# Kernel tuning notes

Hardware: AMD Instinct MI355X
Metric: run time of the kernel (lower is better)

## Reference

```python
import jax, jax.numpy as jnp
import numpy as np

V = 100000   # vocab (emb_size == stoich_size so all 8 branches index safely)
D = 256      # emb_dimension
S = 128      # stoich_dimension
H = 512      # hidden_size
B = 8192     # batch of skip-gram pairs
K = 32       # negative samples per pair
NUM_REGULAR = 60000  # num_regular_words


def _mlp(x, w1, b1, w2, b2):
    # Sequential(Linear(S,H), ReLU, Linear(H,D))
    return jax.nn.relu(x @ w1 + b1) @ w2 + b2


def setup_inputs() -> dict:
    key = jax.random.key(0)
    k = jax.random.split(key, 14)
    initrange = 1.0 / D
    return {
        "pos_u": jax.random.randint(k[0], (B,), 0, V),
        "pos_v": jax.random.randint(k[1], (B,), 0, V),
        "neg_v": jax.random.randint(k[2], (B, K), 0, V),
        "u_emb": jax.random.uniform(k[3], (V, D), jnp.float32, -initrange, initrange),
        "v_emb": jax.random.normal(k[4], (V, D), jnp.float32) * 0.01,
        "stoich": jax.random.uniform(k[5], (V, S), jnp.float32),
        "tw1": jax.random.normal(k[6], (S, H), jnp.float32) * 0.05,
        "tb1": jnp.zeros((H,), jnp.float32),
        "tw2": jax.random.normal(k[7], (H, D), jnp.float32) * 0.05,
        "tb2": jnp.zeros((D,), jnp.float32),
        "cw1": jax.random.normal(k[8], (S, H), jnp.float32) * 0.05,
        "cb1": jnp.zeros((H,), jnp.float32),
        "cw2": jax.random.normal(k[9], (H, D), jnp.float32) * 0.05,
        "cb2": jnp.zeros((D,), jnp.float32),
    }


def _masked_score(emb_u, emb_v, emb_neg_v, u_mask, v_mask, neg_v_mask):
    # pos: [B]
    pos = jnp.clip(jnp.sum(emb_u * emb_v, axis=1), -10.0, 10.0)
    pos = jnp.where(v_mask, 0.0, -jax.nn.log_sigmoid(pos))
    # neg: [B,K] = bmm(emb_neg_v [B,K,D], emb_u [B,D,1])
    neg = jnp.clip(jnp.einsum("bkd,bd->bk", emb_neg_v, emb_u), -10.0, 10.0)
    ls = jnp.where(neg_v_mask, 0.0, jax.nn.log_sigmoid(-neg))
    neg_score = -jnp.sum(ls, axis=1)
    return jnp.where(u_mask, 0.0, pos + neg_score)


def reference(pos_u, pos_v, neg_v, u_emb, v_emb, stoich,
              tw1, tb1, tw2, tb2, cw1, cb1, cw2, cb2):
    emb_u_w = u_emb[pos_u]                 # [B,D]
    emb_v_w = v_emb[pos_v]                 # [B,D]
    emb_neg_v_w = v_emb[neg_v]             # [B,K,D]
    emb_u_m = _mlp(stoich[pos_u], tw1, tb1, tw2, tb2)       # [B,D]
    emb_v_m = _mlp(stoich[pos_v], cw1, cb1, cw2, cb2)       # [B,D]
    emb_neg_v_m = _mlp(stoich[neg_v], cw1, cb1, cw2, cb2)   # [B,K,D]

    u_pairs = [(emb_u_w, pos_u >= NUM_REGULAR), (emb_u_m, pos_u < NUM_REGULAR)]
    v_pairs = [(emb_v_w, pos_v >= NUM_REGULAR), (emb_v_m, pos_v < NUM_REGULAR)]
    n_pairs = [(emb_neg_v_w, neg_v >= NUM_REGULAR), (emb_neg_v_m, neg_v < NUM_REGULAR)]

    total = jnp.zeros((B,), emb_u_w.dtype)
    for eu, um in u_pairs:
        for ev, vm in v_pairs:
            for env, nm in n_pairs:
                total = total + _masked_score(eu, ev, env, um, vm, nm)
    return jnp.mean(total)
```

## Files before the change

kernel.cpp:

```cpp
#include <hip/hip_runtime.h>
#include <hip/hip_bf16.h>
#include <math.h>

#define V_SIZE 100000
#define D_DIM  256
#define S_DIM  128
#define H_DIM  512
#define B_SIZE 8192
#define K_NEG  32
#define NR     60000
#define NMOD   (V_SIZE - NR)

#define TM     48
#define CBLK   834
#define UBLK   171
#define MC_PAD (CBLK * TM)
#define MU_PAD (UBLK * TM)
#define HPAD   516

typedef __attribute__((ext_vector_type(8))) short bf16x8;
typedef __attribute__((ext_vector_type(4))) float f32x4;

static __device__ __forceinline__ short f2bf(float f) {
    unsigned u = __builtin_bit_cast(unsigned, f);
    unsigned r = (u + 0x7fffu + ((u >> 16) & 1u)) >> 16;
    return (short)r;
}

#define N_CONV (MC_PAD * S_DIM / 4)
#define N_XU   (MU_PAD * S_DIM / 4)
#define N_TR   393216

__global__ __launch_bounds__(256) void prep_kernel(
    const float* __restrict__ stoich, const int* __restrict__ pos_u,
    const float* __restrict__ tw1, const float* __restrict__ cw1,
    const float* __restrict__ tw2, const float* __restrict__ cw2,
    short* __restrict__ xbf, short* __restrict__ xu,
    short* __restrict__ W1T_t, short* __restrict__ W1T_c,
    short* __restrict__ W2T_t, short* __restrict__ W2T_c)
{
    int t = blockIdx.x * 256 + threadIdx.x;
    if (t < N_CONV) {
        short4 o = {0, 0, 0, 0};
        if (t < NMOD * S_DIM / 4) {
            const float4 v = ((const float4*)(stoich + (size_t)NR * S_DIM))[t];
            o.x = f2bf(v.x); o.y = f2bf(v.y); o.z = f2bf(v.z); o.w = f2bf(v.w);
        }
        ((short4*)xbf)[t] = o;
    } else if (t < N_CONV + N_XU) {
        int t2 = t - N_CONV;
        int b = t2 >> 5, j = t2 & 31;
        short4 o = {0, 0, 0, 0};
        if (b < B_SIZE) {
            int pu = pos_u[b];
            const float4 v = *(const float4*)(stoich + (size_t)pu * S_DIM + j * 4);
            o.x = f2bf(v.x); o.y = f2bf(v.y); o.z = f2bf(v.z); o.w = f2bf(v.w);
        }
        ((short4*)xu)[t2] = o;
    } else {
        int t3 = t - (N_CONV + N_XU);
        if (t3 < 65536) {
            int n = t3 >> 7, k = t3 & 127;
            W1T_t[t3] = f2bf(tw1[(size_t)k * H_DIM + n]);
        } else if (t3 < 131072) {
            int t4 = t3 - 65536; int n = t4 >> 7, k = t4 & 127;
            W1T_c[t4] = f2bf(cw1[(size_t)k * H_DIM + n]);
        } else if (t3 < 262144) {
            int t4 = t3 - 131072; int n = t4 >> 9, k = t4 & 511;
            W2T_t[t4] = f2bf(tw2[(size_t)k * D_DIM + n]);
        } else if (t3 < N_TR) {
            int t4 = t3 - 262144; int n = t4 >> 9, k = t4 & 511;
            W2T_c[t4] = f2bf(cw2[(size_t)k * D_DIM + n]);
        }
    }
}

__global__ __launch_bounds__(256, 3) void fused_mlp_kernel(
    const short* __restrict__ Xc,  const short* __restrict__ W1c,
    const float* __restrict__ b1c, const short* __restrict__ W2c,
    const float* __restrict__ b2c, float* __restrict__ outc,
    const short* __restrict__ Xu,  const short* __restrict__ W1u,
    const float* __restrict__ b1u, const short* __restrict__ W2u,
    const float* __restrict__ b2u, float* __restrict__ outu)
{
    __shared__ short sH[TM * HPAD];

    const int blk = blockIdx.x;
    const short *A, *W1T, *W2T; const float *b1, *b2; float* out; int m0;
    if (blk < CBLK) { A = Xc; W1T = W1c; b1 = b1c; W2T = W2c; b2 = b2c;
                      out = outc; m0 = blk * TM; }
    else            { A = Xu; W1T = W1u; b1 = b1u; W2T = W2u; b2 = b2u;
                      out = outu; m0 = (blk - CBLK) * TM; }

    const int lane = threadIdx.x & 63;
    const int wv   = threadIdx.x >> 6;
    const int fr   = lane & 15;
    const int q    = lane >> 4;

    const short* Ap = A + (size_t)(m0 + fr) * S_DIM + q * 8;
    bf16x8 af[4][3];
    #pragma unroll
    for (int ks = 0; ks < 4; ++ks)
        #pragma unroll
        for (int mi = 0; mi < 3; ++mi)
            af[ks][mi] = *(const bf16x8*)(Ap + mi * 16 * S_DIM + ks * 32);

    #pragma unroll
    for (int half = 0; half < 2; ++half) {
        const int n0h = wv * 128 + half * 64;
        const short* Bp = W1T + (size_t)(n0h + fr) * S_DIM + q * 8;
        f32x4 acc[3][4] = {};
        #pragma unroll
        for (int ks = 0; ks < 4; ++ks) {
            bf16x8 bfr[4];
            #pragma unroll
            for (int ni = 0; ni < 4; ++ni)
                bfr[ni] = *(const bf16x8*)(Bp + ni * 16 * S_DIM + ks * 32);
            #pragma unroll
            for (int mi = 0; mi < 3; ++mi)
                #pragma unroll
                for (int ni = 0; ni < 4; ++ni)
                    acc[mi][ni] = __builtin_amdgcn_mfma_f32_16x16x32_bf16(
                        af[ks][mi], bfr[ni], acc[mi][ni], 0, 0, 0);
        }
        #pragma unroll
        for (int ni = 0; ni < 4; ++ni) {
            int c = n0h + ni * 16 + fr;
            float bv = b1[c];
            #pragma unroll
            for (int mi = 0; mi < 3; ++mi)
                #pragma unroll
                for (int r = 0; r < 4; ++r)
                    sH[(mi * 16 + q * 4 + r) * HPAD + c] =
                        f2bf(fmaxf(acc[mi][ni][r] + bv, 0.f));
        }
    }
    __syncthreads();

    const short* Bp2 = W2T + (size_t)(wv * 64 + fr) * H_DIM + q * 8;
    f32x4 acc2[3][4] = {};
    bf16x8 bcur[4], bnxt[4], acur[3], anxt[3];

    #define LOAD_B(ks, dst)                                                   \
        _Pragma("unroll")                                                     \
        for (int ni = 0; ni < 4; ++ni)                                        \
            dst[ni] = *(const bf16x8*)(Bp2 + ni * 16 * H_DIM + (ks) * 32);
    #define LOAD_A(ks, dst)                                                   \
        _Pragma("unroll")                                                     \
        for (int mi = 0; mi < 3; ++mi) {                                      \
            const short* hp = &sH[(mi * 16 + fr) * HPAD + (ks) * 32 + q * 8]; \
            short4 lo = *(const short4*)hp;                                   \
            short4 hi = *(const short4*)(hp + 4);                             \
            bf16x8 v;                                                         \
            v[0] = lo.x; v[1] = lo.y; v[2] = lo.z; v[3] = lo.w;               \
            v[4] = hi.x; v[5] = hi.y; v[6] = hi.z; v[7] = hi.w;               \
            dst[mi] = v;                                                      \
        }

    LOAD_B(0, bcur);
    LOAD_A(0, acur);
    #pragma unroll
    for (int ks = 0; ks < 16; ++ks) {
        if (ks < 15) { LOAD_B(ks + 1, bnxt); LOAD_A(ks + 1, anxt); }
        #pragma unroll
        for (int mi = 0; mi < 3; ++mi)
            #pragma unroll
            for (int ni = 0; ni < 4; ++ni)
                acc2[mi][ni] = __builtin_amdgcn_mfma_f32_16x16x32_bf16(
                    acur[mi], bcur[ni], acc2[mi][ni], 0, 0, 0);
        if (ks < 15) {
            #pragma unroll
            for (int i = 0; i < 4; ++i) bcur[i] = bnxt[i];
            #pragma unroll
            for (int i = 0; i < 3; ++i) acur[i] = anxt[i];
        }
    }
    #undef LOAD_A
    #undef LOAD_B

    #pragma unroll
    for (int ni = 0; ni < 4; ++ni) {
        int c = wv * 64 + ni * 16 + fr;
        float bv = b2[c];
        #pragma unroll
        for (int mi = 0; mi < 3; ++mi)
            #pragma unroll
            for (int r = 0; r < 4; ++r) {
                int row = m0 + mi * 16 + q * 4 + r;
                out[(size_t)row * D_DIM + c] = acc2[mi][ni][r] + bv;
            }
    }
}

__device__ __forceinline__ float logsig_fast(float x) {
    float t = __expf(-fabsf(x));
    return fminf(x, 0.f) - __logf(1.f + t);
}
__device__ __forceinline__ float clip10(float x) {
    return fminf(fmaxf(x, -10.f), 10.f);
}
__device__ __forceinline__ float dot4(float4 a, float4 b) {
    return a.x * b.x + a.y * b.y + a.z * b.z + a.w * b.w;
}

__global__ __launch_bounds__(256) void score_kernel(
    const int*   __restrict__ pos_u,
    const int*   __restrict__ pos_v,
    const int*   __restrict__ neg_v,
    const float* __restrict__ u_emb,
    const float* __restrict__ v_emb,
    const float* __restrict__ tab_c,
    const float* __restrict__ Ubuf,
    float* __restrict__ partials)
{
    const int b    = blockIdx.x;
    const int lane = threadIdx.x & 63;
    const int wv   = threadIdx.x >> 6;
    const int g    = lane >> 4;
    const int l    = lane & 15;

    int pu = pos_u[b];
    const float* eup = (pu < NR) ? u_emb + (size_t)pu * D_DIM
                                 : Ubuf  + (size_t)b  * D_DIM;
    float4 eu[4];
    #pragma unroll
    for (int j = 0; j < 4; ++j)
        eu[j] = *(const float4*)(eup + l * 16 + j * 4);

    float part = 0.f;
    const int* nv = neg_v + (size_t)b * K_NEG + wv * 8;

    #pragma unroll
    for (int it = 0; it < 2; ++it) {
        int ix = nv[it * 4 + g];
        const float* rp = (ix < NR) ? v_emb + (size_t)ix * D_DIM
                                    : tab_c + (size_t)(ix - NR) * D_DIM;
        float d = 0.f;
        #pragma unroll
        for (int j = 0; j < 4; ++j)
            d += dot4(eu[j], *(const float4*)(rp + l * 16 + j * 4));
        #pragma unroll
        for (int o = 1; o < 16; o <<= 1) d += __shfl_xor(d, o, 64);
        part -= logsig_fast(-clip10(d));
    }

    if (wv == 0) {
        int pv = pos_v[b];
        const float* rp = (pv < NR) ? v_emb + (size_t)pv * D_DIM
                                    : tab_c + (size_t)(pv - NR) * D_DIM;
        float d = 0.f;
        #pragma unroll
        for (int j = 0; j < 4; ++j)
            d += dot4(eu[j], *(const float4*)(rp + l * 16 + j * 4));
        #pragma unroll
        for (int o = 1; o < 16; o <<= 1) d += __shfl_xor(d, o, 64);
        float term = -logsig_fast(clip10(d));
        if (g == 0) part += term;
    }

    float ws = part;
    #pragma unroll
    for (int o = 32; o; o >>= 1) ws += __shfl_xor(ws, o, 64);
    __shared__ float sp[4];
    if (lane == 0) sp[wv] = ws * 0.0625f;
    __syncthreads();
    if (threadIdx.x == 0)
        partials[b] = sp[0] + sp[1] + sp[2] + sp[3];
}

__global__ __launch_bounds__(256) void reduce_kernel(
    const float* __restrict__ partials, float* __restrict__ out)
{
    float s = 0.f;
    for (int i = threadIdx.x; i < B_SIZE; i += 256) s += partials[i];
    #pragma unroll
    for (int o = 32; o; o >>= 1) s += __shfl_xor(s, o, 64);
    __shared__ float sp[4];
    if ((threadIdx.x & 63) == 0) sp[threadIdx.x >> 6] = s;
    __syncthreads();
    if (threadIdx.x == 0)
        out[0] = (sp[0] + sp[1] + sp[2] + sp[3]) * (2.0f / (float)B_SIZE);
}

extern "C" void kernel_launch(void* const* d_in, const int* in_sizes, int n_in,
                              void* d_out, int out_size, void* d_ws, size_t ws_size,
                              hipStream_t stream) {
    const int*   pos_u  = (const int*)  d_in[0];
    const int*   pos_v  = (const int*)  d_in[1];
    const int*   neg_v  = (const int*)  d_in[2];
    const float* u_emb  = (const float*)d_in[3];
    const float* v_emb  = (const float*)d_in[4];
    const float* stoich = (const float*)d_in[5];
    const float* tw1    = (const float*)d_in[6];
    const float* tb1    = (const float*)d_in[7];
    const float* tw2    = (const float*)d_in[8];
    const float* tb2    = (const float*)d_in[9];
    const float* cw1    = (const float*)d_in[10];
    const float* cb1    = (const float*)d_in[11];
    const float* cw2    = (const float*)d_in[12];
    const float* cb2    = (const float*)d_in[13];
    float* out = (float*)d_out;

    char* ws = (char*)d_ws;
    short* Xbf   = (short*)(ws);
    short* Xu    = (short*)(ws + 10248192);
    short* W1T_t = (short*)(ws + 12349440);
    short* W1T_c = (short*)(ws + 12480512);
    short* W2T_t = (short*)(ws + 12611584);
    short* W2T_c = (short*)(ws + 12873728);
    float* tab_c = (float*)(ws + 13135872);
    float* Ubuf  = (float*)(ws + 54128640);
    float* parts = (float*)(ws + 62533632);

    dim3 blk(256);

    prep_kernel<<<dim3((N_CONV + N_XU + N_TR) / 256), blk, 0, stream>>>(
        stoich, pos_u, tw1, cw1, tw2, cw2,
        Xbf, Xu, W1T_t, W1T_c, W2T_t, W2T_c);

    fused_mlp_kernel<<<dim3(CBLK + UBLK), blk, 0, stream>>>(
        Xbf, W1T_c, cb1, W2T_c, cb2, tab_c,
        Xu,  W1T_t, tb1, W2T_t, tb2, Ubuf);

    score_kernel<<<dim3(B_SIZE), blk, 0, stream>>>(pos_u, pos_v, neg_v,
                                                   u_emb, v_emb, tab_c, Ubuf, parts);
    reduce_kernel<<<dim3(1), blk, 0, stream>>>(parts, out);
}
```

Before: 319.8 us.

## Pre-pack MLP inputs and weights in MFMA fragment order; deepen weight prefetch

The prep kernel now writes the bf16 stoich rows and the transposed weights in the exact per-lane MFMA fragment order, so each wavefront's fragment load becomes one contiguous 1 KB read instead of strided 16-byte reads across rows. The second GEMM prefetches weight fragments three k-steps ahead and issues them before the barrier to hide global latency. The cost is more live registers, which may pressure occupancy under launch_bounds(256,3). The prep kernel's gather writes also become somewhat less regular.

Result: faster. 292.8 us (-8.5%).

```diff
diff --git a/kernel.cpp b/kernel.cpp
--- a/kernel.cpp
+++ b/kernel.cpp
@@ -35,42 +35,54 @@
     const float* __restrict__ stoich, const int* __restrict__ pos_u,
     const float* __restrict__ tw1, const float* __restrict__ cw1,
     const float* __restrict__ tw2, const float* __restrict__ cw2,
-    short* __restrict__ xbf, short* __restrict__ xu,
+    short* __restrict__ xc, short* __restrict__ xu,
     short* __restrict__ W1T_t, short* __restrict__ W1T_c,
     short* __restrict__ W2T_t, short* __restrict__ W2T_c)
 {
     int t = blockIdx.x * 256 + threadIdx.x;
-    if (t < N_CONV) {
+    if (t < N_CONV + N_XU) {
+        const bool cside = t < N_CONV;
+        const int e    = (cside ? t : t - N_CONV) * 4;
+        const int j0   = e & 7;
+        const int lane = (e >> 3) & 63;
+        const int ks   = (e >> 9) & 3;
+        const int rt   = e >> 11;
+        const int row  = rt * 16 + (lane & 15);
+        const int k    = ks * 32 + (lane >> 4) * 8 + j0;
         short4 o = {0, 0, 0, 0};
-        if (t < NMOD * S_DIM / 4) {
-            const float4 v = ((const float4*)(stoich + (size_t)NR * S_DIM))[t];
-            o.x = f2bf(v.x); o.y = f2bf(v.y); o.z = f2bf(v.z); o.w = f2bf(v.w);
-        }
-        ((short4*)xbf)[t] = o;
-    } else if (t < N_CONV + N_XU) {
-        int t2 = t - N_CONV;
-        int b = t2 >> 5, j = t2 & 31;
-        short4 o = {0, 0, 0, 0};
-        if (b < B_SIZE) {
-            int pu = pos_u[b];
-            const float4 v = *(const float4*)(stoich + (size_t)pu * S_DIM + j * 4);
-            o.x = f2bf(v.x); o.y = f2bf(v.y); o.z = f2bf(v.z); o.w = f2bf(v.w);
-        }
-        ((short4*)xu)[t2] = o;
+        if (cside) {
+            if (row < NMOD) {
+                const float4 v = *(const float4*)(stoich + (size_t)(NR + row) * S_DIM + k);
+                o.x = f2bf(v.x); o.y = f2bf(v.y); o.z = f2bf(v.z); o.w = f2bf(v.w);
+            }
+            ((short4*)xc)[t] = o;
+        } else {
+            if (row < B_SIZE) {
+                int pu = pos_u[row];
+                const float4 v = *(const float4*)(stoich + (size_t)pu * S_DIM + k);
+                o.x = f2bf(v.x); o.y = f2bf(v.y); o.z = f2bf(v.z); o.w = f2bf(v.w);
+            }
+            ((short4*)xu)[t - N_CONV] = o;
+        }
     } else {
         int t3 = t - (N_CONV + N_XU);
-        if (t3 < 65536) {
-            int n = t3 >> 7, k = t3 & 127;
-            W1T_t[t3] = f2bf(tw1[(size_t)k * H_DIM + n]);
-        } else if (t3 < 131072) {
-            int t4 = t3 - 65536; int n = t4 >> 7, k = t4 & 127;
-            W1T_c[t4] = f2bf(cw1[(size_t)k * H_DIM + n]);
-        } else if (t3 < 262144) {
-            int t4 = t3 - 131072; int n = t4 >> 9, k = t4 & 511;
-            W2T_t[t4] = f2bf(tw2[(size_t)k * D_DIM + n]);
-        } else if (t3 < N_TR) {
-            int t4 = t3 - 262144; int n = t4 >> 9, k = t4 & 511;
-            W2T_c[t4] = f2bf(cw2[(size_t)k * D_DIM + n]);
+        if (t3 < 131072) {
+            const float* src = (t3 < 65536) ? tw1 : cw1;
+            short*       dst = (t3 < 65536) ? W1T_t : W1T_c;
+            int t4 = t3 & 65535;
+            int j = t4 & 7, lane = (t4 >> 3) & 63;
+            int nt = (t4 >> 9) & 31, ks = (t4 >> 14) & 3;
+            int k = ks * 32 + (lane >> 4) * 8 + j, n = nt * 16 + (lane & 15);
+            dst[t4] = f2bf(src[(size_t)k * H_DIM + n]);
+        } else {
+            int t5 = t3 - 131072;
+            const float* src = (t5 < 131072) ? tw2 : cw2;
+            short*       dst = (t5 < 131072) ? W2T_t : W2T_c;
+            int t4 = t5 & 131071;
+            int j = t4 & 7, lane = (t4 >> 3) & 63;
+            int nt = (t4 >> 9) & 15, ks = (t4 >> 13) & 15;
+            int k = ks * 32 + (lane >> 4) * 8 + j, n = nt * 16 + (lane & 15);
+            dst[t4] = f2bf(src[(size_t)k * D_DIM + n]);
         }
     }
 }
@@ -86,36 +98,37 @@
     __shared__ short sH[TM * HPAD];
 
     const int blk = blockIdx.x;
-    const short *A, *W1T, *W2T; const float *b1, *b2; float* out; int m0;
+    const short *A, *W1T, *W2T; const float *b1, *b2; float* out;
+    int m0, rtb;
     if (blk < CBLK) { A = Xc; W1T = W1c; b1 = b1c; W2T = W2c; b2 = b2c;
-                      out = outc; m0 = blk * TM; }
+                      out = outc; m0 = blk * TM; rtb = blk * 3; }
     else            { A = Xu; W1T = W1u; b1 = b1u; W2T = W2u; b2 = b2u;
-                      out = outu; m0 = (blk - CBLK) * TM; }
+                      out = outu; m0 = (blk - CBLK) * TM; rtb = (blk - CBLK) * 3; }
 
     const int lane = threadIdx.x & 63;
     const int wv   = threadIdx.x >> 6;
     const int fr   = lane & 15;
     const int q    = lane >> 4;
 
-    const short* Ap = A + (size_t)(m0 + fr) * S_DIM + q * 8;
+    const short* Ap = A + (size_t)rtb * 2048 + lane * 8;
     bf16x8 af[4][3];
     #pragma unroll
     for (int ks = 0; ks < 4; ++ks)
         #pragma unroll
         for (int mi = 0; mi < 3; ++mi)
-            af[ks][mi] = *(const bf16x8*)(Ap + mi * 16 * S_DIM + ks * 32);
+            af[ks][mi] = *(const bf16x8*)(Ap + mi * 2048 + ks * 512);
 
     #pragma unroll
     for (int half = 0; half < 2; ++half) {
-        const int n0h = wv * 128 + half * 64;
-        const short* Bp = W1T + (size_t)(n0h + fr) * S_DIM + q * 8;
+        const int nt0 = wv * 8 + half * 4;
+        const short* Bp = W1T + (size_t)nt0 * 512 + lane * 8;
         f32x4 acc[3][4] = {};
         #pragma unroll
         for (int ks = 0; ks < 4; ++ks) {
             bf16x8 bfr[4];
             #pragma unroll
             for (int ni = 0; ni < 4; ++ni)
-                bfr[ni] = *(const bf16x8*)(Bp + ni * 16 * S_DIM + ks * 32);
+                bfr[ni] = *(const bf16x8*)(Bp + ks * 16384 + ni * 512);
             #pragma unroll
             for (int mi = 0; mi < 3; ++mi)
                 #pragma unroll
@@ -125,7 +138,7 @@
         }
         #pragma unroll
         for (int ni = 0; ni < 4; ++ni) {
-            int c = n0h + ni * 16 + fr;
+            int c = (nt0 + ni) * 16 + fr;
             float bv = b1[c];
             #pragma unroll
             for (int mi = 0; mi < 3; ++mi)
@@ -135,16 +148,15 @@
                         f2bf(fmaxf(acc[mi][ni][r] + bv, 0.f));
         }
     }
-    __syncthreads();
-
-    const short* Bp2 = W2T + (size_t)(wv * 64 + fr) * H_DIM + q * 8;
+
+    const short* Bp2 = W2T + (size_t)(wv * 4) * 512 + lane * 8;
     f32x4 acc2[3][4] = {};
-    bf16x8 bcur[4], bnxt[4], acur[3], anxt[3];
+    bf16x8 bA[4], bB[4], bC[4], bD[4], aA[3], aB[3];
 
     #define LOAD_B(ks, dst)                                                   \
         _Pragma("unroll")                                                     \
         for (int ni = 0; ni < 4; ++ni)                                        \
-            dst[ni] = *(const bf16x8*)(Bp2 + ni * 16 * H_DIM + (ks) * 32);
+            dst[ni] = *(const bf16x8*)(Bp2 + (ks) * 8192 + ni * 512);
     #define LOAD_A(ks, dst)                                                   \
         _Pragma("unroll")                                                     \
         for (int mi = 0; mi < 3; ++mi) {                                      \
@@ -157,22 +169,26 @@
             dst[mi] = v;                                                      \
         }
 
-    LOAD_B(0, bcur);
-    LOAD_A(0, acur);
+    LOAD_B(0, bA);
+    LOAD_B(1, bB);
+    LOAD_B(2, bC);
+    __syncthreads();
+    LOAD_A(0, aA);
     #pragma unroll
     for (int ks = 0; ks < 16; ++ks) {
-        if (ks < 15) { LOAD_B(ks + 1, bnxt); LOAD_A(ks + 1, anxt); }
+        if (ks < 13) { LOAD_B(ks + 3, bD); }
+        if (ks < 15) { LOAD_A(ks + 1, aB); }
         #pragma unroll
         for (int mi = 0; mi < 3; ++mi)
             #pragma unroll
             for (int ni = 0; ni < 4; ++ni)
                 acc2[mi][ni] = __builtin_amdgcn_mfma_f32_16x16x32_bf16(
-                    acur[mi], bcur[ni], acc2[mi][ni], 0, 0, 0);
+                    aA[mi], bA[ni], acc2[mi][ni], 0, 0, 0);
         if (ks < 15) {
             #pragma unroll
-            for (int i = 0; i < 4; ++i) bcur[i] = bnxt[i];
-            #pragma unroll
-            for (int i = 0; i < 3; ++i) acur[i] = anxt[i];
+            for (int i = 0; i < 4; ++i) { bA[i] = bB[i]; bB[i] = bC[i]; bC[i] = bD[i]; }
+            #pragma unroll
+            for (int i = 0; i < 3; ++i) aA[i] = aB[i];
         }
     }
     #undef LOAD_A
```
